# Kernel optimization log

Measured on AMD Instinct MI355X. Metric: run time of the kernel, lower is better.

Reference implementation:

```python
import jax, jax.numpy as jnp
import numpy as np

D_MODEL = 64
TEMPER = float(np.power(D_MODEL, 0.5))  # d_model ** temper_value
B, L, DK = 64, 1024, 64
P = 2 * L - 1  # relative position range


def setup_inputs() -> dict:
    key = jax.random.key(0)
    k1, k2, k3, k4, k5 = jax.random.split(key, 5)
    q = jax.random.normal(k1, (B, L, DK), dtype=jnp.float32)
    k = jax.random.normal(k2, (B, L, DK), dtype=jnp.float32)
    v = jax.random.normal(k3, (B, L, DK), dtype=jnp.float32)
    position_dpa = jax.random.normal(k4, (B, P, DK), dtype=jnp.float32)
    attn_mask = jax.random.uniform(k5, (B, L, L)) < 0.1
    return {"q": q, "k": k, "v": v, "position_dpa": position_dpa, "attn_mask": attn_mask}


def reference(q, k, v, position_dpa, attn_mask):
    # q,k,v: [B, L, d]; position_dpa: [B, 2L-1, d]; attn_mask: [B, L, L] bool
    Lq = q.shape[1]
    attn = jnp.einsum('bld,bmd->blm', q, k) / TEMPER            # [B, L, L]
    attn_pos = jnp.einsum('bld,bpd->blp', q, position_dpa) / TEMPER  # [B, L, 2L-1]
    # Replicates batch_stripe(flip(attn_pos.transpose(1,2), -1)).transpose(1,2):
    # bias[b, i, j] = attn_pos[b, L-1-i, i+j]
    i = jnp.arange(Lq)
    rows = (Lq - 1) - i[:, None]                 # [L, 1]
    cols = i[:, None] + i[None, :]               # [L, L], values in [0, 2L-2]
    bias = attn_pos[:, rows, cols]               # [B, L, L]
    attn = attn + bias
    attn = jnp.where(attn_mask, -jnp.inf, attn)
    attn = jax.nn.softmax(attn, axis=-1)
    # dropout is identity in eval mode
    output = jnp.einsum('blm,bmd->bld', attn, v)  # [B, L, d]
    return output, attn
```

## Files before the change

### kernel.cpp

```cpp
#include <hip/hip_runtime.h>

#define BN   64
#define LN   1024
#define DKN  64
#define PN   2047
#define OUT_O_ELEMS ((size_t)BN * LN * DKN)
constexpr float kScale = 0.125f;

typedef short bf16x8 __attribute__((ext_vector_type(8)));
typedef float f32x4  __attribute__((ext_vector_type(4)));

__device__ __forceinline__ unsigned short f2b(float f) {
  return (unsigned short)((__float_as_uint(f) + 0x8000u) >> 16);
}
__device__ __forceinline__ float b2f(unsigned short h) {
  return __uint_as_float(((unsigned)h) << 16);
}
__device__ __forceinline__ unsigned pk2(float x, float y) {
  unsigned lo = (__float_as_uint(x) + 0x8000u) >> 16;
  unsigned hi = (__float_as_uint(y) + 0x8000u) & 0xFFFF0000u;
  return lo | hi;
}

union U8 { unsigned u[4]; bf16x8 v; };

__device__ __forceinline__ bf16x8 pack8(float4 a, float4 b) {
  U8 r;
  r.u[0] = pk2(a.x, a.y); r.u[1] = pk2(a.z, a.w);
  r.u[2] = pk2(b.x, b.y); r.u[3] = pk2(b.z, b.w);
  return r.v;
}

__global__ void flag_init(unsigned* f) { *f = 0u; }

__global__ void flag_scan(const unsigned* __restrict__ mw, unsigned* f) {
  int idx = blockIdx.x * 256 + threadIdx.x;
  unsigned bits = 0;
#pragma unroll
  for (int i = 0; i < 4; ++i) {
    unsigned wv = mw[idx * 4 + i];
    if (wv == 0x3F800000u) bits |= 2u;
    else if (wv > 1u)      bits |= 4u;
  }
  if (bits) atomicOr(f, bits);
}

__global__ __launch_bounds__(256) void convert_f32_bf16(const float4* __restrict__ in,
                                                        uint2* __restrict__ outp) {
  int idx = blockIdx.x * 256 + threadIdx.x;
  float4 a = in[idx];
  outp[idx] = make_uint2(pk2(a.x, a.y), pk2(a.z, a.w));
}

__global__ __launch_bounds__(256) void transpose_v(const float4* __restrict__ vg,
                                                   short* __restrict__ vt) {
  __shared__ float tile[64 * 65];
  const int tid = threadIdx.x;
  const int b  = blockIdx.x >> 4;
  const int mt = blockIdx.x & 15;
  const size_t base = ((size_t)b * 1024 + mt * 64) * 16;
#pragma unroll
  for (int i = 0; i < 4; ++i) {
    int j = tid + (i << 8);
    float4 a = vg[base + j];
    float* d = &tile[(j >> 4) * 65 + ((j & 15) << 2)];
    d[0] = a.x; d[1] = a.y; d[2] = a.z; d[3] = a.w;
  }
  __syncthreads();
#pragma unroll
  for (int i = 0; i < 4; ++i) {
    int j  = tid + (i << 8);
    int d  = j >> 4;
    int mq = (j & 15) << 2;
    unsigned u0 = pk2(tile[(mq + 0) * 65 + d], tile[(mq + 1) * 65 + d]);
    unsigned u1 = pk2(tile[(mq + 2) * 65 + d], tile[(mq + 3) * 65 + d]);
    size_t idx = ((size_t)b * 64 + d) * 1024 + mt * 64 + mq;
    *(uint2*)(vt + idx) = make_uint2(u0, u1);
  }
}

__global__ __launch_bounds__(256, 4)
void attn_kernel(const float* __restrict__ qf, const float* __restrict__ kf,
                 const float* __restrict__ vf, const float* __restrict__ pf,
                 const void* __restrict__ mask, const unsigned* __restrict__ flagp,
                 const short* __restrict__ k16, const short* __restrict__ p16,
                 const short* __restrict__ vt16,
                 float* __restrict__ out) {
  __shared__ short qA[16 * 72];
  __shared__ short qrA[16 * 72];
  __shared__ short E[16 * 1032];
  __shared__ float rowSum[16];

  const int tid  = threadIdx.x;
  const int w    = tid >> 6;
  const int lane = tid & 63;
  const int col  = lane & 15;
  const int quad = lane >> 4;

  int p   = blockIdx.x;
  int xcd = p & 7;
  int qq  = p >> 3;
  int rt  = qq & 63;
  int bh  = qq >> 6;
  const int b  = (bh << 3) | xcd;
  const int l0 = rt << 4;

  unsigned mflag = flagp ? flagp[0] : 0u;
  const int mkind = (mflag & 4u) ? 1 : ((mflag & 2u) ? 2 : 0);

  if (tid < 16) rowSum[tid] = 0.0f;

  {
    const float4* qg = (const float4*)qf;
    int row = tid >> 4, c4 = tid & 15;
    float4 a  = qg[((size_t)b * LN + (l0 + row)) * 16 + c4];
    float4 r_ = qg[((size_t)b * LN + (LN - 1 - l0 - row)) * 16 + c4];
    *(uint2*)&qA[row * 72 + c4 * 4]  = make_uint2(pk2(a.x, a.y), pk2(a.z, a.w));
    *(uint2*)&qrA[row * 72 + c4 * 4] = make_uint2(pk2(r_.x, r_.y), pk2(r_.z, r_.w));
  }
  __syncthreads();

  const bf16x8 aq0 = *(const bf16x8*)&qA[col * 72 + quad * 8];
  const bf16x8 aq1 = *(const bf16x8*)&qA[col * 72 + quad * 8 + 32];
  const bf16x8 ar0 = *(const bf16x8*)&qrA[col * 72 + quad * 8];
  const bf16x8 ar1 = *(const bf16x8*)&qrA[col * 72 + quad * 8 + 32];

  float sumr[4] = {0.f, 0.f, 0.f, 0.f};
  const int moff = (w << 4) + col;
  const size_t mrow0 = (((size_t)b << 10) + (size_t)(l0 + (quad << 2))) << 10;

  if (k16) {
    struct KPM { bf16x8 k0, k1, p00, p01, p10, p11; unsigned m[4]; };
    KPM A, Bf;

    auto LOAD = [&](int t, KPM& o) {
      const int m0 = t << 6, mglob = m0 + moff;
      const short* kr = k16 + ((size_t)b * LN + mglob) * DKN + quad * 8;
      o.k0 = *(const bf16x8*)kr;
      o.k1 = *(const bf16x8*)(kr + 32);
      int g0 = l0 + m0 + moff;
      int g1 = g0 + 16; if (g1 > PN - 1) g1 = PN - 1;
      const short* pr0 = p16 + ((size_t)b * PN + g0) * DKN + quad * 8;
      const short* pr1 = p16 + ((size_t)b * PN + g1) * DKN + quad * 8;
      o.p00 = *(const bf16x8*)pr0;
      o.p01 = *(const bf16x8*)(pr0 + 32);
      o.p10 = *(const bf16x8*)pr1;
      o.p11 = *(const bf16x8*)(pr1 + 32);
      const size_t mi = mrow0 + (size_t)mglob;
      if (mkind == 1) {
        const unsigned char* mp = (const unsigned char*)mask + mi;
#pragma unroll
        for (int r = 0; r < 4; ++r) o.m[r] = mp[(size_t)r << 10];
      } else {
        const unsigned* mp = (const unsigned*)mask + mi;
#pragma unroll
        for (int r = 0; r < 4; ++r) o.m[r] = mp[(size_t)r << 10];
      }
    };

    auto COMP = [&](int t, KPM& o) {
      f32x4 qk = {0.f, 0.f, 0.f, 0.f};
      qk = __builtin_amdgcn_mfma_f32_16x16x32_bf16(aq0, o.k0, qk, 0, 0, 0);
      qk = __builtin_amdgcn_mfma_f32_16x16x32_bf16(aq1, o.k1, qk, 0, 0, 0);
      f32x4 ba = {0.f, 0.f, 0.f, 0.f}, bb = {0.f, 0.f, 0.f, 0.f};
      ba = __builtin_amdgcn_mfma_f32_16x16x32_bf16(ar0, o.p00, ba, 0, 0, 0);
      ba = __builtin_amdgcn_mfma_f32_16x16x32_bf16(ar1, o.p01, ba, 0, 0, 0);
      bb = __builtin_amdgcn_mfma_f32_16x16x32_bf16(ar0, o.p10, bb, 0, 0, 0);
      bb = __builtin_amdgcn_mfma_f32_16x16x32_bf16(ar1, o.p11, bb, 0, 0, 0);
      const int mglob = (t << 6) + moff;
#pragma unroll
      for (int r = 0; r < 4; ++r) {
        int i = (quad << 2) + r;
        int o2 = i + col;
        int srcLane = (lane & 48) | (o2 & 15);
        float va = __shfl(ba[r], srcLane);
        float vb = __shfl(bb[r], srcLane);
        float bias = (o2 < 16) ? va : vb;
        float s = (qk[r] + bias) * kScale;
        float e = o.m[r] ? 0.f : __expf(s);
        unsigned short eb = f2b(e);
        sumr[r] += b2f(eb);
        E[i * 1032 + mglob] = (short)eb;
      }
    };

    LOAD(0, A);
    for (int t = 0; t < 16; t += 2) {
      LOAD(t + 1, Bf);
      COMP(t, A);
      if (t < 14) LOAD(t + 2, A);
      COMP(t + 1, Bf);
    }
  } else {
    for (int t = 0; t < 16; ++t) {
      const int m0 = t << 6, mglob = m0 + moff;
      int g0 = l0 + m0 + moff;
      int g1 = g0 + 16; if (g1 > PN - 1) g1 = PN - 1;
      const float4* kr = (const float4*)(kf + ((size_t)b * LN + mglob) * DKN);
      bf16x8 kb0 = pack8(kr[quad * 2], kr[quad * 2 + 1]);
      bf16x8 kb1 = pack8(kr[8 + quad * 2], kr[9 + quad * 2]);
      const float4* pr0 = (const float4*)(pf + ((size_t)b * PN + g0) * DKN);
      const float4* pr1 = (const float4*)(pf + ((size_t)b * PN + g1) * DKN);
      bf16x8 pb00 = pack8(pr0[quad * 2], pr0[quad * 2 + 1]);
      bf16x8 pb01 = pack8(pr0[8 + quad * 2], pr0[9 + quad * 2]);
      bf16x8 pb10 = pack8(pr1[quad * 2], pr1[quad * 2 + 1]);
      bf16x8 pb11 = pack8(pr1[8 + quad * 2], pr1[9 + quad * 2]);

      f32x4 qk = {0.f, 0.f, 0.f, 0.f};
      qk = __builtin_amdgcn_mfma_f32_16x16x32_bf16(aq0, kb0, qk, 0, 0, 0);
      qk = __builtin_amdgcn_mfma_f32_16x16x32_bf16(aq1, kb1, qk, 0, 0, 0);
      f32x4 ba = {0.f, 0.f, 0.f, 0.f}, bb = {0.f, 0.f, 0.f, 0.f};
      ba = __builtin_amdgcn_mfma_f32_16x16x32_bf16(ar0, pb00, ba, 0, 0, 0);
      ba = __builtin_amdgcn_mfma_f32_16x16x32_bf16(ar1, pb01, ba, 0, 0, 0);
      bb = __builtin_amdgcn_mfma_f32_16x16x32_bf16(ar0, pb10, bb, 0, 0, 0);
      bb = __builtin_amdgcn_mfma_f32_16x16x32_bf16(ar1, pb11, bb, 0, 0, 0);

#pragma unroll
      for (int r = 0; r < 4; ++r) {
        int i = (quad << 2) + r;
        int o2 = i + col;
        int srcLane = (lane & 48) | (o2 & 15);
        float va = __shfl(ba[r], srcLane);
        float vb = __shfl(bb[r], srcLane);
        float bias = (o2 < 16) ? va : vb;
        float s = (qk[r] + bias) * kScale;
        size_t mi = mrow0 + ((size_t)r << 10) + (size_t)mglob;
        unsigned mu = (mkind == 1) ? (unsigned)((const unsigned char*)mask)[mi]
                                   : ((const unsigned*)mask)[mi];
        float e = mu ? 0.f : __expf(s);
        unsigned short eb = f2b(e);
        sumr[r] += b2f(eb);
        E[i * 1032 + mglob] = (short)eb;
      }
    }
  }

#pragma unroll
  for (int r = 0; r < 4; ++r) {
    float vsum = sumr[r];
    vsum += __shfl_xor(vsum, 1);
    vsum += __shfl_xor(vsum, 2);
    vsum += __shfl_xor(vsum, 4);
    vsum += __shfl_xor(vsum, 8);
    if (col == 0) atomicAdd(&rowSum[(quad << 2) + r], vsum);
  }
  __syncthreads();

  f32x4 acc = {0.f, 0.f, 0.f, 0.f};
  const int drow = moff;
  float* outA = out + OUT_O_ELEMS;
  const size_t aBase = (((size_t)b << 10) + (size_t)l0) << 10;

  auto WROW = [&](int t) {
    float inv = 1.0f / rowSum[t];
    const ushort4 ev = *(const ushort4*)&E[t * 1032 + (tid << 2)];
    float4 o4;
    o4.x = b2f(ev.x) * inv;
    o4.y = b2f(ev.y) * inv;
    o4.z = b2f(ev.z) * inv;
    o4.w = b2f(ev.w) * inv;
    *(float4*)&outA[aBase + ((size_t)t << 10) + (size_t)(tid << 2)] = o4;
  };

  if (vt16) {
    const short* vbase = vt16 + ((size_t)b * 64 + drow) * 1024 + quad * 8;
    bf16x8 v0A = *(const bf16x8*)vbase;
    bf16x8 v1A = *(const bf16x8*)(vbase + 32);
    bf16x8 v0B, v1B;
    for (int t = 0; t < 16; t += 2) {
      { const short* vr = vbase + ((t + 1) << 6);
        v0B = *(const bf16x8*)vr; v1B = *(const bf16x8*)(vr + 32); }
      { const int m0 = t << 6;
        bf16x8 ea0 = *(const bf16x8*)&E[col * 1032 + m0 + quad * 8];
        bf16x8 ea1 = *(const bf16x8*)&E[col * 1032 + m0 + 32 + quad * 8];
        acc = __builtin_amdgcn_mfma_f32_16x16x32_bf16(ea0, v0A, acc, 0, 0, 0);
        acc = __builtin_amdgcn_mfma_f32_16x16x32_bf16(ea1, v1A, acc, 0, 0, 0);
        WROW(t); }
      if (t < 14) { const short* vr = vbase + ((t + 2) << 6);
        v0A = *(const bf16x8*)vr; v1A = *(const bf16x8*)(vr + 32); }
      { const int m0 = (t + 1) << 6;
        bf16x8 ea0 = *(const bf16x8*)&E[col * 1032 + m0 + quad * 8];
        bf16x8 ea1 = *(const bf16x8*)&E[col * 1032 + m0 + 32 + quad * 8];
        acc = __builtin_amdgcn_mfma_f32_16x16x32_bf16(ea0, v0B, acc, 0, 0, 0);
        acc = __builtin_amdgcn_mfma_f32_16x16x32_bf16(ea1, v1B, acc, 0, 0, 0);
        WROW(t + 1); }
    }
  } else {
    for (int t = 0; t < 16; ++t) {
      const int m0 = t << 6;
      const float* vc = vf + ((size_t)b * LN + m0) * DKN + drow;
      U8 t0, t1;
#pragma unroll
      for (int j = 0; j < 4; ++j) {
        t0.u[j] = pk2(vc[(quad * 8 + 2 * j) * 64],      vc[(quad * 8 + 2 * j + 1) * 64]);
        t1.u[j] = pk2(vc[(32 + quad * 8 + 2 * j) * 64], vc[(32 + quad * 8 + 2 * j + 1) * 64]);
      }
      bf16x8 ea0 = *(const bf16x8*)&E[col * 1032 + m0 + quad * 8];
      bf16x8 ea1 = *(const bf16x8*)&E[col * 1032 + m0 + 32 + quad * 8];
      acc = __builtin_amdgcn_mfma_f32_16x16x32_bf16(ea0, t0.v, acc, 0, 0, 0);
      acc = __builtin_amdgcn_mfma_f32_16x16x32_bf16(ea1, t1.v, acc, 0, 0, 0);
    }
    for (int t = 0; t < 16; ++t) WROW(t);
  }

#pragma unroll
  for (int r = 0; r < 4; ++r) {
    int i = (quad << 2) + r;
    out[(((size_t)b << 10) + (size_t)(l0 + i)) * 64 + drow] = acc[r] * (1.0f / rowSum[i]);
  }
}

extern "C" void kernel_launch(void* const* d_in, const int* in_sizes, int n_in,
                              void* d_out, int out_size, void* d_ws, size_t ws_size,
                              hipStream_t stream) {
  const float* q   = (const float*)d_in[0];
  const float* k   = (const float*)d_in[1];
  const float* v   = (const float*)d_in[2];
  const float* pos = (const float*)d_in[3];
  const void* mask = d_in[4];
  float* out = (float*)d_out;

  unsigned* flag = nullptr;
  if (ws_size >= 256) {
    flag = (unsigned*)d_ws;
    flag_init<<<1, 1, 0, stream>>>(flag);
    flag_scan<<<64, 256, 0, stream>>>((const unsigned*)mask, flag);
  }

  const size_t kElems  = (size_t)BN * LN * DKN;
  const size_t pElems  = (size_t)BN * PN * DKN;
  const size_t offK    = 256;
  const size_t offP    = offK + kElems * 2;
  const size_t offVT   = offP + pElems * 2;
  const size_t wsNeed  = offVT + kElems * 2;

  short *k16 = nullptr, *p16 = nullptr, *vt16 = nullptr;
  if (ws_size >= wsNeed) {
    char* base = (char*)d_ws;
    k16  = (short*)(base + offK);
    p16  = (short*)(base + offP);
    vt16 = (short*)(base + offVT);
    convert_f32_bf16<<<(int)(kElems / 1024), 256, 0, stream>>>((const float4*)k,   (uint2*)k16);
    convert_f32_bf16<<<(int)(pElems / 1024), 256, 0, stream>>>((const float4*)pos, (uint2*)p16);
    transpose_v<<<BN * 16, 256, 0, stream>>>((const float4*)v, vt16);
  }

  attn_kernel<<<BN * (LN / 16), 256, 0, stream>>>(q, k, v, pos, mask, flag,
                                                  k16, p16, vt16, out);
}
```

Measured before the change: 705.7 us.

## Shrink LDS, swizzle E buffer, fuse conversions, compute row sums in PV loop

Removes the Q staging buffers and the rowSum shared array, loading Q directly from global into registers, and stores E unpadded with an XOR swizzle to avoid bank conflicts. Row sums are now accumulated from the bf16 E values read during the PV loop and reduced with shuffles, replacing the shared-memory atomics. The attention-matrix write is moved after the PV loop and uses nontemporal stores, mask loads become nontemporal, the launch bound raises occupancy to 8 blocks, and the two conversion kernels are merged into one launch. Higher occupancy may increase register pressure, and moving the attention write to the end removes its overlap with the MFMA work.

```diff
diff --git a/kernel.cpp b/kernel.cpp
--- a/kernel.cpp
+++ b/kernel.cpp
@@ -45,11 +45,19 @@
   if (bits) atomicOr(f, bits);
 }
 
-__global__ __launch_bounds__(256) void convert_f32_bf16(const float4* __restrict__ in,
-                                                        uint2* __restrict__ outp) {
+__global__ __launch_bounds__(256) void convert2_f32_bf16(const float4* __restrict__ a,
+                                                         uint2* __restrict__ oa, int na,
+                                                         const float4* __restrict__ bsrc,
+                                                         uint2* __restrict__ ob) {
   int idx = blockIdx.x * 256 + threadIdx.x;
-  float4 a = in[idx];
-  outp[idx] = make_uint2(pk2(a.x, a.y), pk2(a.z, a.w));
+  if (idx < na) {
+    float4 x = a[idx];
+    oa[idx] = make_uint2(pk2(x.x, x.y), pk2(x.z, x.w));
+  } else {
+    int j = idx - na;
+    float4 x = bsrc[j];
+    ob[j] = make_uint2(pk2(x.x, x.y), pk2(x.z, x.w));
+  }
 }
 
 __global__ __launch_bounds__(256) void transpose_v(const float4* __restrict__ vg,
@@ -79,17 +87,14 @@
   }
 }
 
-__global__ __launch_bounds__(256, 4)
+__global__ __launch_bounds__(256, 8)
 void attn_kernel(const float* __restrict__ qf, const float* __restrict__ kf,
                  const float* __restrict__ vf, const float* __restrict__ pf,
                  const void* __restrict__ mask, const unsigned* __restrict__ flagp,
                  const short* __restrict__ k16, const short* __restrict__ p16,
                  const short* __restrict__ vt16,
                  float* __restrict__ out) {
-  __shared__ short qA[16 * 72];
-  __shared__ short qrA[16 * 72];
-  __shared__ short E[16 * 1032];
-  __shared__ float rowSum[16];
+  __shared__ short E[16 * 1024];
 
   const int tid  = threadIdx.x;
   const int w    = tid >> 6;
@@ -108,24 +113,14 @@
   unsigned mflag = flagp ? flagp[0] : 0u;
   const int mkind = (mflag & 4u) ? 1 : ((mflag & 2u) ? 2 : 0);
 
-  if (tid < 16) rowSum[tid] = 0.0f;
-
-  {
-    const float4* qg = (const float4*)qf;
-    int row = tid >> 4, c4 = tid & 15;
-    float4 a  = qg[((size_t)b * LN + (l0 + row)) * 16 + c4];
-    float4 r_ = qg[((size_t)b * LN + (LN - 1 - l0 - row)) * 16 + c4];
-    *(uint2*)&qA[row * 72 + c4 * 4]  = make_uint2(pk2(a.x, a.y), pk2(a.z, a.w));
-    *(uint2*)&qrA[row * 72 + c4 * 4] = make_uint2(pk2(r_.x, r_.y), pk2(r_.z, r_.w));
-  }
-  __syncthreads();
-
-  const bf16x8 aq0 = *(const bf16x8*)&qA[col * 72 + quad * 8];
-  const bf16x8 aq1 = *(const bf16x8*)&qA[col * 72 + quad * 8 + 32];
-  const bf16x8 ar0 = *(const bf16x8*)&qrA[col * 72 + quad * 8];
-  const bf16x8 ar1 = *(const bf16x8*)&qrA[col * 72 + quad * 8 + 32];
-
-  float sumr[4] = {0.f, 0.f, 0.f, 0.f};
+  const float4* qg = (const float4*)qf;
+  const size_t qrow  = ((size_t)b * LN + (size_t)(l0 + col)) * 16 + (size_t)(quad * 2);
+  const size_t qrrow = ((size_t)b * LN + (size_t)(LN - 1 - l0 - col)) * 16 + (size_t)(quad * 2);
+  const bf16x8 aq0 = pack8(qg[qrow],      qg[qrow + 1]);
+  const bf16x8 aq1 = pack8(qg[qrow + 8],  qg[qrow + 9]);
+  const bf16x8 ar0 = pack8(qg[qrrow],     qg[qrrow + 1]);
+  const bf16x8 ar1 = pack8(qg[qrrow + 8], qg[qrrow + 9]);
+
   const int moff = (w << 4) + col;
   const size_t mrow0 = (((size_t)b << 10) + (size_t)(l0 + (quad << 2))) << 10;
 
@@ -150,11 +145,11 @@
       if (mkind == 1) {
         const unsigned char* mp = (const unsigned char*)mask + mi;
 #pragma unroll
-        for (int r = 0; r < 4; ++r) o.m[r] = mp[(size_t)r << 10];
+        for (int r = 0; r < 4; ++r) o.m[r] = __builtin_nontemporal_load(mp + ((size_t)r << 10));
       } else {
         const unsigned* mp = (const unsigned*)mask + mi;
 #pragma unroll
-        for (int r = 0; r < 4; ++r) o.m[r] = mp[(size_t)r << 10];
+        for (int r = 0; r < 4; ++r) o.m[r] = __builtin_nontemporal_load(mp + ((size_t)r << 10));
       }
     };
 
@@ -178,9 +173,7 @@
         float bias = (o2 < 16) ? va : vb;
         float s = (qk[r] + bias) * kScale;
         float e = o.m[r] ? 0.f : __expf(s);
-        unsigned short eb = f2b(e);
-        sumr[r] += b2f(eb);
-        E[i * 1032 + mglob] = (short)eb;
+        E[i * 1024 + (mglob ^ ((i & 7) << 3))] = (short)f2b(e);
       }
     };
 
@@ -228,38 +221,24 @@
         unsigned mu = (mkind == 1) ? (unsigned)((const unsigned char*)mask)[mi]
                                    : ((const unsigned*)mask)[mi];
         float e = mu ? 0.f : __expf(s);
-        unsigned short eb = f2b(e);
-        sumr[r] += b2f(eb);
-        E[i * 1032 + mglob] = (short)eb;
+        E[i * 1024 + (mglob ^ ((i & 7) << 3))] = (short)f2b(e);
       }
     }
   }
-
-#pragma unroll
-  for (int r = 0; r < 4; ++r) {
-    float vsum = sumr[r];
-    vsum += __shfl_xor(vsum, 1);
-    vsum += __shfl_xor(vsum, 2);
-    vsum += __shfl_xor(vsum, 4);
-    vsum += __shfl_xor(vsum, 8);
-    if (col == 0) atomicAdd(&rowSum[(quad << 2) + r], vsum);
-  }
   __syncthreads();
 
   f32x4 acc = {0.f, 0.f, 0.f, 0.f};
+  float sLo = 0.f, sHi = 0.f;
   const int drow = moff;
-  float* outA = out + OUT_O_ELEMS;
-  const size_t aBase = (((size_t)b << 10) + (size_t)l0) << 10;
-
-  auto WROW = [&](int t) {
-    float inv = 1.0f / rowSum[t];
-    const ushort4 ev = *(const ushort4*)&E[t * 1032 + (tid << 2)];
-    float4 o4;
-    o4.x = b2f(ev.x) * inv;
-    o4.y = b2f(ev.y) * inv;
-    o4.z = b2f(ev.z) * inv;
-    o4.w = b2f(ev.w) * inv;
-    *(float4*)&outA[aBase + ((size_t)t << 10) + (size_t)(tid << 2)] = o4;
+  const int esw  = (col & 7) << 3;
+
+  auto EAT = [&](bf16x8 ev) {
+    U8 u; u.v = ev;
+#pragma unroll
+    for (int j = 0; j < 4; ++j) {
+      sLo += __uint_as_float(u.u[j] << 16);
+      sHi += __uint_as_float(u.u[j] & 0xFFFF0000u);
+    }
   };
 
   if (vt16) {
@@ -271,19 +250,19 @@
       { const short* vr = vbase + ((t + 1) << 6);
         v0B = *(const bf16x8*)vr; v1B = *(const bf16x8*)(vr + 32); }
       { const int m0 = t << 6;
-        bf16x8 ea0 = *(const bf16x8*)&E[col * 1032 + m0 + quad * 8];
-        bf16x8 ea1 = *(const bf16x8*)&E[col * 1032 + m0 + 32 + quad * 8];
+        bf16x8 ea0 = *(const bf16x8*)&E[col * 1024 + ((m0 + quad * 8) ^ esw)];
+        bf16x8 ea1 = *(const bf16x8*)&E[col * 1024 + ((m0 + 32 + quad * 8) ^ esw)];
         acc = __builtin_amdgcn_mfma_f32_16x16x32_bf16(ea0, v0A, acc, 0, 0, 0);
         acc = __builtin_amdgcn_mfma_f32_16x16x32_bf16(ea1, v1A, acc, 0, 0, 0);
-        WROW(t); }
+        EAT(ea0); EAT(ea1); }
       if (t < 14) { const short* vr = vbase + ((t + 2) << 6);
         v0A = *(const bf16x8*)vr; v1A = *(const bf16x8*)(vr + 32); }
       { const int m0 = (t + 1) << 6;
-        bf16x8 ea0 = *(const bf16x8*)&E[col * 1032 + m0 + quad * 8];
-        bf16x8 ea1 = *(const bf16x8*)&E[col * 1032 + m0 + 32 + quad * 8];
+        bf16x8 ea0 = *(const bf16x8*)&E[col * 1024 + ((m0 + quad * 8) ^ esw)];
+        bf16x8 ea1 = *(const bf16x8*)&E[col * 1024 + ((m0 + 32 + quad * 8) ^ esw)];
         acc = __builtin_amdgcn_mfma_f32_16x16x32_bf16(ea0, v0B, acc, 0, 0, 0);
         acc = __builtin_amdgcn_mfma_f32_16x16x32_bf16(ea1, v1B, acc, 0, 0, 0);
-        WROW(t + 1); }
+        EAT(ea0); EAT(ea1); }
     }
   } else {
     for (int t = 0; t < 16; ++t) {
@@ -295,18 +274,37 @@
         t0.u[j] = pk2(vc[(quad * 8 + 2 * j) * 64],      vc[(quad * 8 + 2 * j + 1) * 64]);
         t1.u[j] = pk2(vc[(32 + quad * 8 + 2 * j) * 64], vc[(32 + quad * 8 + 2 * j + 1) * 64]);
       }
-      bf16x8 ea0 = *(const bf16x8*)&E[col * 1032 + m0 + quad * 8];
-      bf16x8 ea1 = *(const bf16x8*)&E[col * 1032 + m0 + 32 + quad * 8];
+      bf16x8 ea0 = *(const bf16x8*)&E[col * 1024 + ((m0 + quad * 8) ^ esw)];
+      bf16x8 ea1 = *(const bf16x8*)&E[col * 1024 + ((m0 + 32 + quad * 8) ^ esw)];
       acc = __builtin_amdgcn_mfma_f32_16x16x32_bf16(ea0, t0.v, acc, 0, 0, 0);
       acc = __builtin_amdgcn_mfma_f32_16x16x32_bf16(ea1, t1.v, acc, 0, 0, 0);
-    }
-    for (int t = 0; t < 16; ++t) WROW(t);
-  }
+      EAT(ea0); EAT(ea1);
+    }
+  }
+
+  float s = sLo + sHi;
+  s += __shfl_xor(s, 16);
+  s += __shfl_xor(s, 32);
+  const float invS = 1.0f / s;
 
 #pragma unroll
   for (int r = 0; r < 4; ++r) {
     int i = (quad << 2) + r;
-    out[(((size_t)b << 10) + (size_t)(l0 + i)) * 64 + drow] = acc[r] * (1.0f / rowSum[i]);
+    float invi = __shfl(invS, (lane & 48) | i);
+    out[(((size_t)b << 10) + (size_t)(l0 + i)) * 64 + drow] = acc[r] * invi;
+  }
+
+  float* outA = out + OUT_O_ELEMS;
+  const size_t aBase = (((size_t)b << 10) + (size_t)l0) << 10;
+  for (int t = 0; t < 16; ++t) {
+    float inv = __shfl(invS, (lane & 48) | t);
+    const ushort4 ev = *(const ushort4*)&E[t * 1024 + ((tid << 2) ^ ((t & 7) << 3))];
+    f32x4 o4;
+    o4[0] = b2f(ev.x) * inv;
+    o4[1] = b2f(ev.y) * inv;
+    o4[2] = b2f(ev.z) * inv;
+    o4[3] = b2f(ev.w) * inv;
+    __builtin_nontemporal_store(o4, (f32x4*)&outA[aBase + ((size_t)t << 10) + (size_t)(tid << 2)]);
   }
 }
 
@@ -340,8 +338,10 @@
     k16  = (short*)(base + offK);
     p16  = (short*)(base + offP);
     vt16 = (short*)(base + offVT);
-    convert_f32_bf16<<<(int)(kElems / 1024), 256, 0, stream>>>((const float4*)k,   (uint2*)k16);
-    convert_f32_bf16<<<(int)(pElems / 1024), 256, 0, stream>>>((const float4*)pos, (uint2*)p16);
+    const int na = (int)(kElems / 4);
+    const int nb = (int)(pElems / 4);
+    convert2_f32_bf16<<<(na + nb) / 256, 256, 0, stream>>>((const float4*)k, (uint2*)k16, na,
+                                                           (const float4*)pos, (uint2*)p16);
     transpose_v<<<BN * 16, 256, 0, stream>>>((const float4*)v, vt16);
   }
 
```

Result: no change. 698.0 us (-1.1%).
